# Optimization experiments

Hardware: AMD Instinct MI355X
Metric: run time of the kernel (lower is better)

The kernel has to match this reference:

```python
import jax, jax.numpy as jnp
import numpy as np

NUM_HEADS = 4
LN_EPS = 1e-5
ALPHA_SCALE = 2.0


def setup_inputs() -> dict:
    key = jax.random.key(0)
    ks = jax.random.split(key, 8)
    bs, C, H, W = 64, 256, 56, 56
    T, D = 6, 192
    HW = H * W
    w = lambda k, shape: (jax.random.normal(k, shape, jnp.float32) * 0.02)
    return {
        "features": jax.random.normal(ks[0], (bs, C, H, W), jnp.float32),
        "tokens": jax.random.normal(ks[1], (T, bs, D), jnp.float32),
        # mlp: Linear(HW -> T)
        "mlp_w": w(ks[2], (T, HW)), "mlp_b": jnp.zeros((T,), jnp.float32),
        # q: Linear(D -> C)
        "q_w": w(ks[3], (C, D)), "q_b": jnp.zeros((C,), jnp.float32),
        # alpha: Linear(D -> C)
        "alpha_w": w(ks[4], (C, D)), "alpha_b": jnp.zeros((C,), jnp.float32),
        # proj: Linear(C -> D)
        "proj_w": w(ks[5], (D, C)), "proj_b": jnp.zeros((D,), jnp.float32),
        "ln_g": jnp.ones((D,), jnp.float32), "ln_b": jnp.zeros((D,), jnp.float32),
    }


def reference(features, tokens, mlp_w, mlp_b, q_w, q_b,
              alpha_w, alpha_b, proj_w, proj_b, ln_g, ln_b):
    bs, C, H, W = features.shape
    T, _, D = tokens.shape
    h = NUM_HEADS
    dh = C // h
    HW = H * W
    scale = dh ** -0.5

    f = features.reshape(bs, C, HW)

    # mlp branch: Linear over HW -> [bs, C, T] -> permute to [T, bs, C]
    t_sum = jnp.einsum('bcn,tn->tbc', f, mlp_w) + mlp_b[:, None, None]

    # attn branch: few tokens attend over H*W feature map (k reused as v)
    q = jnp.einsum('tbd,cd->tbc', tokens, q_w) + q_b          # [T, bs, C]
    q = q.reshape(T, bs, h, dh).transpose(1, 2, 0, 3)         # [bs, h, T, dh]
    k = f.reshape(bs, h, dh, HW)                              # [bs, h, dh, HW]
    attn = jnp.einsum('bhtd,bhdn->bhtn', q, k) * scale        # [bs, h, T, HW]
    a = jax.nn.softmax(attn, axis=-1)
    attn_out = jnp.einsum('bhtn,bhdn->bhtd', a, k)            # [bs, h, T, dh]
    t_a = attn_out.transpose(2, 0, 1, 3).reshape(T, bs, C)
    t_sum = t_sum + t_a

    # dynamic gate: h_sigmoid(alpha(tokens)) * 2.0
    alp = jnp.clip(jnp.einsum('tbd,cd->tbc', tokens, alpha_w) + alpha_b + 3.0,
                   0.0, 6.0) / 6.0 * ALPHA_SCALE              # [T, bs, C]
    t_sum = t_sum * alp

    # proj + residual + LayerNorm (post-norm, drop_path rate 0 -> identity)
    t_sum = jnp.einsum('tbc,dc->tbd', t_sum, proj_w) + proj_b  # [T, bs, D]
    tok = tokens + t_sum
    mu = tok.mean(-1, keepdims=True)
    var = ((tok - mu) ** 2).mean(-1, keepdims=True)
    tok = (tok - mu) * jax.lax.rsqrt(var + LN_EPS) * ln_g + ln_b

    return tok, attn.reshape(bs, h, T, H, W)
```

## Files before the change

kernel.cpp:

```cpp
#include <hip/hip_runtime.h>
#include <hip/hip_bf16.h>

constexpr int BS = 64, C = 256, NH = 4, DH = 64, T = 6, D = 192;
constexpr int HW = 3136;
constexpr int NT = 112;
constexpr int S = 7, CPB = 4;
constexpr int PNF = 136;
constexpr int PNS = 116;
constexpr int QP = 72;
constexpr float SCALE = 0.125f;
constexpr float LN_EPS = 1e-5f;

typedef short bf16x8 __attribute__((ext_vector_type(8)));
typedef float f32x4 __attribute__((ext_vector_type(4)));

__device__ inline unsigned short f2bf(float x) {
    union { float f; unsigned u; } v; v.f = x;
    unsigned r = v.u + 0x7FFFu + ((v.u >> 16) & 1u);
    return (unsigned short)(r >> 16);
}

__global__ __launch_bounds__(256) void qalpha_kernel(
    const float* __restrict__ tokens,
    const float* __restrict__ q_w,
    const float* __restrict__ q_b,
    const float* __restrict__ alpha_w,
    const float* __restrict__ alpha_b,
    float* __restrict__ q_ws,
    float* __restrict__ alp_ws)
{
    int b = blockIdx.x;
    int c = threadIdx.x;
    __shared__ float tok_s[T][D];
    for (int i = c; i < T * (D / 4); i += 256) {
        int t = i / (D / 4), v = i % (D / 4);
        *(float4*)&tok_s[t][4 * v] =
            *(const float4*)&tokens[((size_t)t * BS + b) * D + 4 * v];
    }
    __syncthreads();

    const float4* qr = (const float4*)(q_w + (size_t)c * D);
    const float4* ar = (const float4*)(alpha_w + (size_t)c * D);
    float accq[T] = {0, 0, 0, 0, 0, 0};
    float acca[T] = {0, 0, 0, 0, 0, 0};
    for (int v = 0; v < D / 4; ++v) {
        float4 qw4 = qr[v], aw4 = ar[v];
#pragma unroll
        for (int t = 0; t < T; ++t) {
            float4 t4 = *(const float4*)&tok_s[t][4 * v];
            accq[t] += qw4.x * t4.x + qw4.y * t4.y + qw4.z * t4.z + qw4.w * t4.w;
            acca[t] += aw4.x * t4.x + aw4.y * t4.y + aw4.z * t4.z + aw4.w * t4.w;
        }
    }
    float qb = q_b[c], ab = alpha_b[c];
#pragma unroll
    for (int t = 0; t < T; ++t) {
        size_t idx = ((size_t)t * BS + b) * C + c;
        q_ws[idx] = accq[t] + qb;
        float aa = acca[t] + ab + 3.0f;
        alp_ws[idx] = fminf(fmaxf(aa, 0.0f), 6.0f) * (2.0f / 6.0f);
    }
}

__global__ __launch_bounds__(384) void fused_attn_mlp(
    const float* __restrict__ feat,
    const float* __restrict__ mlp_w,
    const float* __restrict__ q_ws,
    float* __restrict__ out_attn,
    float* __restrict__ o_part,
    float* __restrict__ mlp_part,
    float* __restrict__ ml_part)
{
    int bh = blockIdx.x / S, sp = blockIdx.x % S;
    int b = bh / NH, h = bh % NH;
    int tid = threadIdx.x;
    int wave = tid >> 6, lane = tid & 63;
    int col = lane & 15, quad = lane >> 4;

    __shared__ unsigned short fch[DH][PNF];
    __shared__ unsigned short pw[16][PNF];
    __shared__ unsigned short qs[16][QP];
    __shared__ float st[T][PNS];
    __shared__ float m_s[T], l_s[T], al_s[T];

    for (int i = tid; i < 16 * PNF; i += 384) pw[i / PNF][i % PNF] = 0;
    for (int i = tid; i < DH * 24; i += 384) fch[i / 24][112 + (i % 24)] = 0;
    for (int i = tid; i < 16 * QP; i += 384) qs[i / QP][i % QP] = 0;
    if (tid < T) { m_s[tid] = -3e38f; l_s[tid] = 0.f; }
    __syncthreads();
    for (int i = tid; i < T * DH; i += 384) {
        int t = i / DH, c2 = i % DH;
        qs[t][c2] = f2bf(q_ws[((size_t)t * BS + b) * C + h * DH + c2]);
    }

    const float* fbase = feat + ((size_t)b * C + h * DH) * HW;
    float* obase = out_attn + ((size_t)bh * T) * HW;

    f32x4 accPW = {0.f, 0.f, 0.f, 0.f};
    __syncthreads();

    for (int cc = 0; cc < CPB; ++cc) {
        const int n0 = (sp * CPB + cc) * NT;
        for (int i = tid; i < DH * (NT / 4); i += 384) {
            int c2 = i / (NT / 4), v = i % (NT / 4);
            float4 f4 = *(const float4*)&fbase[(size_t)c2 * HW + n0 + 4 * v];
            unsigned lo = (unsigned)f2bf(f4.x) | ((unsigned)f2bf(f4.y) << 16);
            unsigned hi = (unsigned)f2bf(f4.z) | ((unsigned)f2bf(f4.w) << 16);
            *(uint2*)&fch[c2][4 * v] = make_uint2(lo, hi);
        }
        for (int i = tid; i < T * (NT / 4); i += 384) {
            int t = i / (NT / 4), v = i % (NT / 4);
            float4 f4 = *(const float4*)&mlp_w[(size_t)t * HW + n0 + 4 * v];
            unsigned lo = (unsigned)f2bf(f4.x) | ((unsigned)f2bf(f4.y) << 16);
            unsigned hi = (unsigned)f2bf(f4.z) | ((unsigned)f2bf(f4.w) << 16);
            *(uint2*)&pw[6 + t][4 * v] = make_uint2(lo, hi);
        }
        __syncthreads();

        for (int tile = wave; tile < 7; tile += 6) {
            bf16x8 a0 = *(const bf16x8*)&qs[col][quad * 8];
            bf16x8 a1 = *(const bf16x8*)&qs[col][32 + quad * 8];
            bf16x8 b0, b1;
#pragma unroll
            for (int j = 0; j < 8; ++j) {
                b0[j] = (short)fch[quad * 8 + j][tile * 16 + col];
                b1[j] = (short)fch[32 + quad * 8 + j][tile * 16 + col];
            }
            f32x4 acc = {0.f, 0.f, 0.f, 0.f};
            acc = __builtin_amdgcn_mfma_f32_16x16x32_bf16(a0, b0, acc, 0, 0, 0);
            acc = __builtin_amdgcn_mfma_f32_16x16x32_bf16(a1, b1, acc, 0, 0, 0);
#pragma unroll
            for (int reg = 0; reg < 4; ++reg) {
                int r = quad * 4 + reg;
                if (r < 6) st[r][tile * 16 + col] = acc[reg] * SCALE;
            }
        }
        __syncthreads();

        {
            int t = wave;
            float v0 = st[t][lane];
            float v1 = (lane + 64 < NT) ? st[t][lane + 64] : -3e38f;
            float mloc = fmaxf(v0, v1);
#pragma unroll
            for (int off = 32; off; off >>= 1) mloc = fmaxf(mloc, __shfl_down(mloc, off));
            mloc = __shfl(mloc, 0);
            float m_old = m_s[t], m_new = fmaxf(m_old, mloc);
            float p0 = __expf(v0 - m_new);
            float p1 = (lane + 64 < NT) ? __expf(v1 - m_new) : 0.f;
            pw[t][lane] = f2bf(p0);
            if (lane + 64 < NT) pw[t][lane + 64] = f2bf(p1);
            float ssum = p0 + p1;
#pragma unroll
            for (int off = 32; off; off >>= 1) ssum += __shfl_down(ssum, off);
            if (lane == 0) {
                float alpha = __expf(m_old - m_new);
                l_s[t] = l_s[t] * alpha + ssum;
                m_s[t] = m_new;
                al_s[t] = alpha;
            }
            if (lane < NT / 4) {
                *(float4*)&obase[(size_t)t * HW + n0 + 4 * lane] =
                    *(const float4*)&st[t][4 * lane];
            }
        }
        __syncthreads();

        if (wave < 4) {
            float alpha = (col < 6) ? al_s[col] : 1.0f;
            accPW *= alpha;
#pragma unroll
            for (int ks = 0; ks < 4; ++ks) {
                bf16x8 af = *(const bf16x8*)&fch[wave * 16 + col][ks * 32 + quad * 8];
                bf16x8 bf = *(const bf16x8*)&pw[col][ks * 32 + quad * 8];
                accPW = __builtin_amdgcn_mfma_f32_16x16x32_bf16(af, bf, accPW, 0, 0, 0);
            }
        }
        __syncthreads();
    }

    if (wave < 4) {
#pragma unroll
        for (int reg = 0; reg < 4; ++reg) {
            int c2 = wave * 16 + quad * 4 + reg;
            if (col < 6) {
                o_part[((size_t)blockIdx.x * T + col) * DH + c2] = accPW[reg];
            } else if (col < 12) {
                mlp_part[((size_t)blockIdx.x * T + (col - 6)) * DH + c2] = accPW[reg];
            }
        }
    }
    if (tid < 2 * T) {
        int t = tid >> 1;
        ml_part[((size_t)blockIdx.x * T + t) * 2 + (tid & 1)] =
            (tid & 1) ? l_s[t] : m_s[t];
    }
}

__global__ __launch_bounds__(256) void merge_proj_ln_kernel(
    const float* __restrict__ o_part,
    const float* __restrict__ mlp_part,
    const float* __restrict__ ml_part,
    const float* __restrict__ mlp_b,
    const float* __restrict__ alp_ws,
    const float* __restrict__ tokens,
    const float* __restrict__ proj_w,
    const float* __restrict__ proj_b,
    const float* __restrict__ ln_g,
    const float* __restrict__ ln_b,
    float* __restrict__ out_tok)
{
    int tb = blockIdx.x;
    int t = tb / BS, b = tb % BS;
    int tid = threadIdx.x;
    __shared__ float g_s[C];
    __shared__ float r1[4], r2[4];

    {
        int c = tid;
        int h = c >> 6, cl = c & 63;
        int bh = b * NH + h;
        float m[S], l[S];
        float M = -3e38f;
#pragma unroll
        for (int s = 0; s < S; ++s) {
            size_t blk = (size_t)(bh * S + s);
            m[s] = ml_part[(blk * T + t) * 2 + 0];
            l[s] = ml_part[(blk * T + t) * 2 + 1];
            M = fmaxf(M, m[s]);
        }
        float L = 0.f, O = 0.f, MLP = 0.f;
#pragma unroll
        for (int s = 0; s < S; ++s) {
            float w = __expf(m[s] - M);
            size_t blk = (size_t)(bh * S + s);
            size_t pidx = (blk * T + t) * DH + cl;
            L += l[s] * w;
            O += o_part[pidx] * w;
            MLP += mlp_part[pidx];
        }
        size_t idx = (size_t)tb * C + c;
        g_s[c] = (MLP + mlp_b[t] + O / L) * alp_ws[idx];
    }
    __syncthreads();

    if (tid < D) {
        int d = tid;
        float acc = proj_b[d] + tokens[(size_t)tb * D + d];
        const float4* pr = (const float4*)(proj_w + (size_t)d * C);
#pragma unroll 8
        for (int v = 0; v < C / 4; ++v) {
            float4 w4 = pr[v];
            float4 g4 = *(const float4*)&g_s[4 * v];
            acc += w4.x * g4.x + w4.y * g4.y + w4.z * g4.z + w4.w * g4.w;
        }

        float s1 = acc, s2 = acc * acc;
#pragma unroll
        for (int off = 32; off; off >>= 1) { s1 += __shfl_down(s1, off); s2 += __shfl_down(s2, off); }
        int wv = d >> 6, lane = d & 63;
        if (lane == 0) { r1[wv] = s1; r2[wv] = s2; }
        __syncthreads();
        float sum1 = r1[0] + r1[1] + r1[2];
        float sum2 = r2[0] + r2[1] + r2[2];
        float mu = sum1 * (1.0f / D);
        float var = sum2 * (1.0f / D) - mu * mu;
        float inv = rsqrtf(var + LN_EPS);
        out_tok[(size_t)tb * D + d] = (acc - mu) * inv * ln_g[d] + ln_b[d];
    } else {
        __syncthreads();
    }
}

extern "C" void kernel_launch(void* const* d_in, const int* in_sizes, int n_in,
                              void* d_out, int out_size, void* d_ws, size_t ws_size,
                              hipStream_t stream) {
    const float* features = (const float*)d_in[0];
    const float* tokens   = (const float*)d_in[1];
    const float* mlp_w    = (const float*)d_in[2];
    const float* mlp_b    = (const float*)d_in[3];
    const float* q_w      = (const float*)d_in[4];
    const float* q_b      = (const float*)d_in[5];
    const float* alpha_w  = (const float*)d_in[6];
    const float* alpha_b  = (const float*)d_in[7];
    const float* proj_w   = (const float*)d_in[8];
    const float* proj_b   = (const float*)d_in[9];
    const float* ln_g     = (const float*)d_in[10];
    const float* ln_b     = (const float*)d_in[11];

    float* out_tok  = (float*)d_out;
    float* out_attn = (float*)d_out + T * BS * D;

    constexpr int NBLK = BS * NH * S;
    float* q_ws     = (float*)d_ws;
    float* alp_ws   = q_ws + T * BS * C;
    float* ml_part  = alp_ws + T * BS * C;
    float* o_part   = ml_part + NBLK * T * 2;
    float* mlp_part = o_part + NBLK * T * DH;

    qalpha_kernel<<<BS, 256, 0, stream>>>(
        tokens, q_w, q_b, alpha_w, alpha_b, q_ws, alp_ws);

    fused_attn_mlp<<<NBLK, 384, 0, stream>>>(
        features, mlp_w, q_ws, out_attn, o_part, mlp_part, ml_part);

    merge_proj_ln_kernel<<<T * BS, 256, 0, stream>>>(
        o_part, mlp_part, ml_part, mlp_b, alp_ws, tokens,
        proj_w, proj_b, ln_g, ln_b, out_tok);
}
```

Measured before the change: 355.4 us.

## Fuse q/alpha projections into consumers and register-prefetch feature chunks

Removes the separate qalpha kernel. Each attention block now computes its own q head slice from tokens, and the alpha gate is computed inside the merge/proj/LN kernel. The main loop prefetches the next feature and mlp_w chunk into registers before converting and storing to LDS, so global latency overlaps with the MFMA and softmax work. __syncthreads is replaced by an lgkmcnt-only wait plus barrier, so outstanding global loads do not block the barrier. In exchange, q_w work is duplicated across the 7 spatial splits, alpha_w work is spread over 384 blocks, and more registers are needed for the prefetch.

```diff
diff --git a/kernel.cpp b/kernel.cpp
--- a/kernel.cpp
+++ b/kernel.cpp
@@ -20,52 +20,24 @@
     return (unsigned short)(r >> 16);
 }
 
-__global__ __launch_bounds__(256) void qalpha_kernel(
+__device__ inline void st_bf8(unsigned short* dst, float4 p) {
+    unsigned lo = (unsigned)f2bf(p.x) | ((unsigned)f2bf(p.y) << 16);
+    unsigned hi = (unsigned)f2bf(p.z) | ((unsigned)f2bf(p.w) << 16);
+    *(uint2*)dst = make_uint2(lo, hi);
+}
+
+__device__ inline void wg_barrier_lgkm() {
+    asm volatile("s_waitcnt lgkmcnt(0)" ::: "memory");
+    __builtin_amdgcn_s_barrier();
+    asm volatile("" ::: "memory");
+}
+
+__global__ __launch_bounds__(384) void fused_attn_mlp(
+    const float* __restrict__ feat,
+    const float* __restrict__ mlp_w,
     const float* __restrict__ tokens,
     const float* __restrict__ q_w,
     const float* __restrict__ q_b,
-    const float* __restrict__ alpha_w,
-    const float* __restrict__ alpha_b,
-    float* __restrict__ q_ws,
-    float* __restrict__ alp_ws)
-{
-    int b = blockIdx.x;
-    int c = threadIdx.x;
-    __shared__ float tok_s[T][D];
-    for (int i = c; i < T * (D / 4); i += 256) {
-        int t = i / (D / 4), v = i % (D / 4);
-        *(float4*)&tok_s[t][4 * v] =
-            *(const float4*)&tokens[((size_t)t * BS + b) * D + 4 * v];
-    }
-    __syncthreads();
-
-    const float4* qr = (const float4*)(q_w + (size_t)c * D);
-    const float4* ar = (const float4*)(alpha_w + (size_t)c * D);
-    float accq[T] = {0, 0, 0, 0, 0, 0};
-    float acca[T] = {0, 0, 0, 0, 0, 0};
-    for (int v = 0; v < D / 4; ++v) {
-        float4 qw4 = qr[v], aw4 = ar[v];
-#pragma unroll
-        for (int t = 0; t < T; ++t) {
-            float4 t4 = *(const float4*)&tok_s[t][4 * v];
-            accq[t] += qw4.x * t4.x + qw4.y * t4.y + qw4.z * t4.z + qw4.w * t4.w;
-            acca[t] += aw4.x * t4.x + aw4.y * t4.y + aw4.z * t4.z + aw4.w * t4.w;
-        }
-    }
-    float qb = q_b[c], ab = alpha_b[c];
-#pragma unroll
-    for (int t = 0; t < T; ++t) {
-        size_t idx = ((size_t)t * BS + b) * C + c;
-        q_ws[idx] = accq[t] + qb;
-        float aa = acca[t] + ab + 3.0f;
-        alp_ws[idx] = fminf(fmaxf(aa, 0.0f), 6.0f) * (2.0f / 6.0f);
-    }
-}
-
-__global__ __launch_bounds__(384) void fused_attn_mlp(
-    const float* __restrict__ feat,
-    const float* __restrict__ mlp_w,
-    const float* __restrict__ q_ws,
     float* __restrict__ out_attn,
     float* __restrict__ o_part,
     float* __restrict__ mlp_part,
@@ -83,39 +55,68 @@
     __shared__ float st[T][PNS];
     __shared__ float m_s[T], l_s[T], al_s[T];
 
-    for (int i = tid; i < 16 * PNF; i += 384) pw[i / PNF][i % PNF] = 0;
-    for (int i = tid; i < DH * 24; i += 384) fch[i / 24][112 + (i % 24)] = 0;
-    for (int i = tid; i < 16 * QP; i += 384) qs[i / QP][i % QP] = 0;
-    if (tid < T) { m_s[tid] = -3e38f; l_s[tid] = 0.f; }
-    __syncthreads();
-    for (int i = tid; i < T * DH; i += 384) {
-        int t = i / DH, c2 = i % DH;
-        qs[t][c2] = f2bf(q_ws[((size_t)t * BS + b) * C + h * DH + c2]);
-    }
-
     const float* fbase = feat + ((size_t)b * C + h * DH) * HW;
     float* obase = out_attn + ((size_t)bh * T) * HW;
 
+    float qacc;
+    {
+        const float4* tr = (const float4*)&tokens[((size_t)wave * BS + b) * D];
+        const float4* qr = (const float4*)&q_w[(size_t)(h * DH + lane) * D];
+        float acc = 0.f;
+#pragma unroll 4
+        for (int v = 0; v < D / 4; ++v) {
+            float4 t4 = tr[v], w4 = qr[v];
+            acc += t4.x * w4.x + t4.y * w4.y + t4.z * w4.z + t4.w * w4.w;
+        }
+        qacc = acc + q_b[h * DH + lane];
+    }
+
+    float4 pf0, pf1, pf2, pf3, pf4, pm;
+    {
+        const int n0 = sp * CPB * NT;
+        pf0 = *(const float4*)&fbase[(size_t)(tid / 28) * HW + n0 + 4 * (tid % 28)];
+        pf1 = *(const float4*)&fbase[(size_t)((tid + 384) / 28) * HW + n0 + 4 * ((tid + 384) % 28)];
+        pf2 = *(const float4*)&fbase[(size_t)((tid + 768) / 28) * HW + n0 + 4 * ((tid + 768) % 28)];
+        pf3 = *(const float4*)&fbase[(size_t)((tid + 1152) / 28) * HW + n0 + 4 * ((tid + 1152) % 28)];
+        if (tid < 256)
+            pf4 = *(const float4*)&fbase[(size_t)((tid + 1536) / 28) * HW + n0 + 4 * ((tid + 1536) % 28)];
+        if (tid < 168)
+            pm = *(const float4*)&mlp_w[(size_t)(tid / 28) * HW + n0 + 4 * (tid % 28)];
+    }
+
+    for (int i = tid; i < 16 * PNF; i += 384) pw[i / PNF][i % PNF] = 0;
+    for (int i = tid; i < DH * 16; i += 384) fch[i / 16][112 + (i % 16)] = 0;
+    if (tid < T) { m_s[tid] = -3e38f; l_s[tid] = 0.f; }
+    qs[wave][lane] = f2bf(qacc);
+
     f32x4 accPW = {0.f, 0.f, 0.f, 0.f};
-    __syncthreads();
-
+    wg_barrier_lgkm();
+
+#pragma unroll 1
     for (int cc = 0; cc < CPB; ++cc) {
         const int n0 = (sp * CPB + cc) * NT;
-        for (int i = tid; i < DH * (NT / 4); i += 384) {
-            int c2 = i / (NT / 4), v = i % (NT / 4);
-            float4 f4 = *(const float4*)&fbase[(size_t)c2 * HW + n0 + 4 * v];
-            unsigned lo = (unsigned)f2bf(f4.x) | ((unsigned)f2bf(f4.y) << 16);
-            unsigned hi = (unsigned)f2bf(f4.z) | ((unsigned)f2bf(f4.w) << 16);
-            *(uint2*)&fch[c2][4 * v] = make_uint2(lo, hi);
-        }
-        for (int i = tid; i < T * (NT / 4); i += 384) {
-            int t = i / (NT / 4), v = i % (NT / 4);
-            float4 f4 = *(const float4*)&mlp_w[(size_t)t * HW + n0 + 4 * v];
-            unsigned lo = (unsigned)f2bf(f4.x) | ((unsigned)f2bf(f4.y) << 16);
-            unsigned hi = (unsigned)f2bf(f4.z) | ((unsigned)f2bf(f4.w) << 16);
-            *(uint2*)&pw[6 + t][4 * v] = make_uint2(lo, hi);
-        }
-        __syncthreads();
+
+        st_bf8(&fch[tid / 28][4 * (tid % 28)], pf0);
+        st_bf8(&fch[(tid + 384) / 28][4 * ((tid + 384) % 28)], pf1);
+        st_bf8(&fch[(tid + 768) / 28][4 * ((tid + 768) % 28)], pf2);
+        st_bf8(&fch[(tid + 1152) / 28][4 * ((tid + 1152) % 28)], pf3);
+        if (tid < 256)
+            st_bf8(&fch[(tid + 1536) / 28][4 * ((tid + 1536) % 28)], pf4);
+        if (tid < 168)
+            st_bf8(&pw[6 + tid / 28][4 * (tid % 28)], pm);
+
+        if (cc + 1 < CPB) {
+            const int n1 = n0 + NT;
+            pf0 = *(const float4*)&fbase[(size_t)(tid / 28) * HW + n1 + 4 * (tid % 28)];
+            pf1 = *(const float4*)&fbase[(size_t)((tid + 384) / 28) * HW + n1 + 4 * ((tid + 384) % 28)];
+            pf2 = *(const float4*)&fbase[(size_t)((tid + 768) / 28) * HW + n1 + 4 * ((tid + 768) % 28)];
+            pf3 = *(const float4*)&fbase[(size_t)((tid + 1152) / 28) * HW + n1 + 4 * ((tid + 1152) % 28)];
+            if (tid < 256)
+                pf4 = *(const float4*)&fbase[(size_t)((tid + 1536) / 28) * HW + n1 + 4 * ((tid + 1536) % 28)];
+            if (tid < 168)
+                pm = *(const float4*)&mlp_w[(size_t)(tid / 28) * HW + n1 + 4 * (tid % 28)];
+        }
+        wg_barrier_lgkm();
 
         for (int tile = wave; tile < 7; tile += 6) {
             bf16x8 a0 = *(const bf16x8*)&qs[col][quad * 8];
@@ -135,7 +136,7 @@
                 if (r < 6) st[r][tile * 16 + col] = acc[reg] * SCALE;
             }
         }
-        __syncthreads();
+        wg_barrier_lgkm();
 
         {
             int t = wave;
@@ -164,7 +165,7 @@
                     *(const float4*)&st[t][4 * lane];
             }
         }
-        __syncthreads();
+        wg_barrier_lgkm();
 
         if (wave < 4) {
             float alpha = (col < 6) ? al_s[col] : 1.0f;
@@ -176,7 +177,7 @@
                 accPW = __builtin_amdgcn_mfma_f32_16x16x32_bf16(af, bf, accPW, 0, 0, 0);
             }
         }
-        __syncthreads();
+        wg_barrier_lgkm();
     }
 
     if (wave < 4) {
@@ -202,7 +203,8 @@
     const float* __restrict__ mlp_part,
     const float* __restrict__ ml_part,
     const float* __restrict__ mlp_b,
-    const float* __restrict__ alp_ws,
+    const float* __restrict__ alpha_w,
+    const float* __restrict__ alpha_b,
     const float* __restrict__ tokens,
     const float* __restrict__ proj_w,
     const float* __restrict__ proj_b,
@@ -213,11 +215,27 @@
     int tb = blockIdx.x;
     int t = tb / BS, b = tb % BS;
     int tid = threadIdx.x;
+    __shared__ float tok_s[D];
     __shared__ float g_s[C];
     __shared__ float r1[4], r2[4];
 
+    if (tid < D / 4)
+        *(float4*)&tok_s[4 * tid] = *(const float4*)&tokens[(size_t)tb * D + 4 * tid];
+    __syncthreads();
+
     {
         int c = tid;
+        const float4* ar = (const float4*)(alpha_w + (size_t)c * D);
+        float acca = 0.f;
+#pragma unroll 8
+        for (int v = 0; v < D / 4; ++v) {
+            float4 w4 = ar[v];
+            float4 t4 = *(const float4*)&tok_s[4 * v];
+            acca += w4.x * t4.x + w4.y * t4.y + w4.z * t4.z + w4.w * t4.w;
+        }
+        float aa = acca + alpha_b[c] + 3.0f;
+        float gate = fminf(fmaxf(aa, 0.0f), 6.0f) * (2.0f / 6.0f);
+
         int h = c >> 6, cl = c & 63;
         int bh = b * NH + h;
         float m[S], l[S];
@@ -239,14 +257,13 @@
             O += o_part[pidx] * w;
             MLP += mlp_part[pidx];
         }
-        size_t idx = (size_t)tb * C + c;
-        g_s[c] = (MLP + mlp_b[t] + O / L) * alp_ws[idx];
+        g_s[c] = (MLP + mlp_b[t] + O / L) * gate;
     }
     __syncthreads();
 
     if (tid < D) {
         int d = tid;
-        float acc = proj_b[d] + tokens[(size_t)tb * D + d];
+        float acc = proj_b[d] + tok_s[d];
         const float4* pr = (const float4*)(proj_w + (size_t)d * C);
 #pragma unroll 8
         for (int v = 0; v < C / 4; ++v) {
@@ -292,19 +309,14 @@
     float* out_attn = (float*)d_out + T * BS * D;
 
     constexpr int NBLK = BS * NH * S;
-    float* q_ws     = (float*)d_ws;
-    float* alp_ws   = q_ws + T * BS * C;
-    float* ml_part  = alp_ws + T * BS * C;
+    float* ml_part  = (float*)d_ws;
     float* o_part   = ml_part + NBLK * T * 2;
     float* mlp_part = o_part + NBLK * T * DH;
 
-    qalpha_kernel<<<BS, 256, 0, stream>>>(
-        tokens, q_w, q_b, alpha_w, alpha_b, q_ws, alp_ws);
-
     fused_attn_mlp<<<NBLK, 384, 0, stream>>>(
-        features, mlp_w, q_ws, out_attn, o_part, mlp_part, ml_part);
+        features, mlp_w, tokens, q_w, q_b, out_attn, o_part, mlp_part, ml_part);
 
     merge_proj_ln_kernel<<<T * BS, 256, 0, stream>>>(
-        o_part, mlp_part, ml_part, mlp_b, alp_ws, tokens,
+        o_part, mlp_part, ml_part, mlp_b, alpha_w, alpha_b, tokens,
         proj_w, proj_b, ln_g, ln_b, out_tok);
 }
```

Result: slower. 384.5 us (+8.2%).

## Register double-buffer feature chunk prefetch and use lgkm-only barriers

Applied to the files above, without the earlier changes.

Issues the global loads for the next two feature/mlp_w chunks into registers before processing the current chunk, so load latency overlaps the MFMA and softmax work. Replaces __syncthreads with a barrier that waits only on LDS counters, so outstanding global prefetches are not drained at each barrier. Also changes the split from 7 blocks of 4 chunks to 4 blocks of 7 chunks per (b,h) and sets a minimum of 6 blocks per CU in launch bounds. The prefetch buffers raise register pressure, and fewer blocks lowers parallelism across the grid.

```diff
diff --git a/kernel.cpp b/kernel.cpp
--- a/kernel.cpp
+++ b/kernel.cpp
@@ -4,7 +4,7 @@
 constexpr int BS = 64, C = 256, NH = 4, DH = 64, T = 6, D = 192;
 constexpr int HW = 3136;
 constexpr int NT = 112;
-constexpr int S = 7, CPB = 4;
+constexpr int S = 4, CPB = 7;
 constexpr int PNF = 136;
 constexpr int PNS = 116;
 constexpr int QP = 72;
@@ -18,6 +18,18 @@
     union { float f; unsigned u; } v; v.f = x;
     unsigned r = v.u + 0x7FFFu + ((v.u >> 16) & 1u);
     return (unsigned short)(r >> 16);
+}
+
+__device__ inline void st_bf8(unsigned short* dst, float4 p) {
+    unsigned lo = (unsigned)f2bf(p.x) | ((unsigned)f2bf(p.y) << 16);
+    unsigned hi = (unsigned)f2bf(p.z) | ((unsigned)f2bf(p.w) << 16);
+    *(uint2*)dst = make_uint2(lo, hi);
+}
+
+__device__ inline void wg_barrier_lgkm() {
+    asm volatile("s_waitcnt lgkmcnt(0)" ::: "memory");
+    __builtin_amdgcn_s_barrier();
+    asm volatile("" ::: "memory");
 }
 
 __global__ __launch_bounds__(256) void qalpha_kernel(
@@ -62,7 +74,9 @@
     }
 }
 
-__global__ __launch_bounds__(384) void fused_attn_mlp(
+struct PF { float4 f0, f1, f2, f3, f4, m; };
+
+__global__ __launch_bounds__(384, 6) void fused_attn_mlp(
     const float* __restrict__ feat,
     const float* __restrict__ mlp_w,
     const float* __restrict__ q_ws,
@@ -83,39 +97,51 @@
     __shared__ float st[T][PNS];
     __shared__ float m_s[T], l_s[T], al_s[T];
 
-    for (int i = tid; i < 16 * PNF; i += 384) pw[i / PNF][i % PNF] = 0;
-    for (int i = tid; i < DH * 24; i += 384) fch[i / 24][112 + (i % 24)] = 0;
-    for (int i = tid; i < 16 * QP; i += 384) qs[i / QP][i % QP] = 0;
-    if (tid < T) { m_s[tid] = -3e38f; l_s[tid] = 0.f; }
-    __syncthreads();
-    for (int i = tid; i < T * DH; i += 384) {
-        int t = i / DH, c2 = i % DH;
-        qs[t][c2] = f2bf(q_ws[((size_t)t * BS + b) * C + h * DH + c2]);
-    }
-
     const float* fbase = feat + ((size_t)b * C + h * DH) * HW;
     float* obase = out_attn + ((size_t)bh * T) * HW;
 
+    const int o0 = (tid / 28) * HW + 4 * (tid % 28);
+    const int o1 = ((tid + 384) / 28) * HW + 4 * ((tid + 384) % 28);
+    const int o2 = ((tid + 768) / 28) * HW + 4 * ((tid + 768) % 28);
+    const int o3 = ((tid + 1152) / 28) * HW + 4 * ((tid + 1152) % 28);
+    const int o4 = ((tid + 1536) / 28) * HW + 4 * ((tid + 1536) % 28);
+
+    auto pf_issue = [&](PF& p, int n0) {
+        p.f0 = *(const float4*)&fbase[o0 + n0];
+        p.f1 = *(const float4*)&fbase[o1 + n0];
+        p.f2 = *(const float4*)&fbase[o2 + n0];
+        p.f3 = *(const float4*)&fbase[o3 + n0];
+        if (tid < 256) p.f4 = *(const float4*)&fbase[o4 + n0];
+        if (tid < 168) p.m  = *(const float4*)&mlp_w[o0 + n0];
+    };
+    auto pf_commit = [&](const PF& p) {
+        st_bf8(&fch[tid / 28][4 * (tid % 28)], p.f0);
+        st_bf8(&fch[(tid + 384) / 28][4 * ((tid + 384) % 28)], p.f1);
+        st_bf8(&fch[(tid + 768) / 28][4 * ((tid + 768) % 28)], p.f2);
+        st_bf8(&fch[(tid + 1152) / 28][4 * ((tid + 1152) % 28)], p.f3);
+        if (tid < 256) st_bf8(&fch[(tid + 1536) / 28][4 * ((tid + 1536) % 28)], p.f4);
+        if (tid < 168) st_bf8(&pw[6 + tid / 28][4 * (tid % 28)], p.m);
+    };
+
+    const int nsp = sp * CPB * NT;
+    PF A, B;
+    pf_issue(A, nsp);
+    pf_issue(B, nsp + NT);
+
+    for (int i = tid; i < 16 * PNF; i += 384) pw[i / PNF][i % PNF] = 0;
+    for (int i = tid; i < DH * 16; i += 384) fch[i / 16][112 + (i % 16)] = 0;
+    if (tid < T) { m_s[tid] = -3e38f; l_s[tid] = 0.f; }
+    qs[wave][lane] = f2bf(q_ws[((size_t)wave * BS + b) * C + h * DH + lane]);
+
     f32x4 accPW = {0.f, 0.f, 0.f, 0.f};
-    __syncthreads();
-
-    for (int cc = 0; cc < CPB; ++cc) {
-        const int n0 = (sp * CPB + cc) * NT;
-        for (int i = tid; i < DH * (NT / 4); i += 384) {
-            int c2 = i / (NT / 4), v = i % (NT / 4);
-            float4 f4 = *(const float4*)&fbase[(size_t)c2 * HW + n0 + 4 * v];
-            unsigned lo = (unsigned)f2bf(f4.x) | ((unsigned)f2bf(f4.y) << 16);
-            unsigned hi = (unsigned)f2bf(f4.z) | ((unsigned)f2bf(f4.w) << 16);
-            *(uint2*)&fch[c2][4 * v] = make_uint2(lo, hi);
-        }
-        for (int i = tid; i < T * (NT / 4); i += 384) {
-            int t = i / (NT / 4), v = i % (NT / 4);
-            float4 f4 = *(const float4*)&mlp_w[(size_t)t * HW + n0 + 4 * v];
-            unsigned lo = (unsigned)f2bf(f4.x) | ((unsigned)f2bf(f4.y) << 16);
-            unsigned hi = (unsigned)f2bf(f4.z) | ((unsigned)f2bf(f4.w) << 16);
-            *(uint2*)&pw[6 + t][4 * v] = make_uint2(lo, hi);
-        }
-        __syncthreads();
+    wg_barrier_lgkm();
+
+    auto chunk_body = [&](int cc, PF& P) {
+        const int n0 = nsp + cc * NT;
+
+        pf_commit(P);
+        if (cc + 2 < CPB) pf_issue(P, n0 + 2 * NT);
+        wg_barrier_lgkm();
 
         for (int tile = wave; tile < 7; tile += 6) {
             bf16x8 a0 = *(const bf16x8*)&qs[col][quad * 8];
@@ -135,7 +161,7 @@
                 if (r < 6) st[r][tile * 16 + col] = acc[reg] * SCALE;
             }
         }
-        __syncthreads();
+        wg_barrier_lgkm();
 
         {
             int t = wave;
@@ -164,7 +190,7 @@
                     *(const float4*)&st[t][4 * lane];
             }
         }
-        __syncthreads();
+        wg_barrier_lgkm();
 
         if (wave < 4) {
             float alpha = (col < 6) ? al_s[col] : 1.0f;
@@ -176,7 +202,13 @@
                 accPW = __builtin_amdgcn_mfma_f32_16x16x32_bf16(af, bf, accPW, 0, 0, 0);
             }
         }
-        __syncthreads();
+        wg_barrier_lgkm();
+    };
+
+#pragma unroll 1
+    for (int cc = 0; cc < CPB; cc += 2) {
+        chunk_body(cc, A);
+        if (cc + 1 < CPB) chunk_body(cc + 1, B);
     }
 
     if (wave < 4) {
```

New measurement: 442.4 us. 24.5% more time.
